# Optimization experiments

Measured on AMD Instinct MI355X. Metric: run time of the kernel, lower is better.

Reference implementation:

```python
import jax, jax.numpy as jnp
import numpy as np

C = 512
NUM_HEADS = 8
HEAD_DIM = C // NUM_HEADS


def setup_inputs() -> dict:
    key = jax.random.key(0)
    ks = jax.random.split(key, 5)
    B, H, W = 4, 48, 48
    x = jax.random.normal(ks[0], (B, C, H, W), dtype=jnp.float32)
    # 1x1 conv weights == dense matrices over channel dim
    Wqkv = jax.random.normal(ks[1], (3 * C, C), dtype=jnp.float32) * (1.0 / np.sqrt(C))
    bqkv = jax.random.normal(ks[2], (3 * C,), dtype=jnp.float32) * 0.01
    Wout = jax.random.normal(ks[3], (C, C), dtype=jnp.float32) * (1.0 / np.sqrt(C))
    bout = jax.random.normal(ks[4], (C,), dtype=jnp.float32) * 0.01
    return {"x": x, "Wqkv": Wqkv, "bqkv": bqkv, "Wout": Wout, "bout": bout}


def reference(x, Wqkv, bqkv, Wout, bout):
    B, Cc, H, W = x.shape
    S = H * W
    # qkv 1x1 conv: [B, 3C, H, W] -> reshape (B, 3, heads, head_dim, S)
    qkv = jnp.einsum('bchw,oc->bohw', x, Wqkv) + bqkv[None, :, None, None]
    qkv = qkv.reshape(B, 3, NUM_HEADS, HEAD_DIM, S)
    q, k, v = qkv[:, 0], qkv[:, 1], qkv[:, 2]  # [B, h, d, S]
    # tokens along S: q^T k, scaled softmax
    scale = HEAD_DIM ** -0.5
    attn = jnp.einsum('bhds,bhdt->bhst', q, k) * scale  # [B, h, S, S]
    attn = jax.nn.softmax(attn, axis=-1)
    out = jnp.einsum('bhst,bhdt->bhds', attn, v)  # [B, h, d, S]
    out = out.reshape(B, Cc, H, W)
    out = jnp.einsum('bchw,oc->bohw', out, Wout) + bout[None, :, None, None]
    return out
```

## Files before the change

kernel.cpp:

```cpp
#include <hip/hip_runtime.h>

#define S_LEN 2304
#define CDIM  512
#define NHEAD 8

typedef __attribute__((ext_vector_type(4)))  float f32x4;
typedef __attribute__((ext_vector_type(16))) float f32x16;
typedef __attribute__((ext_vector_type(8)))  _Float16 f16x8;
typedef __attribute__((ext_vector_type(2)))  __fp16 fp16x2r;
typedef _Float16 h16;

#define QSCALE 0.18033688011112042f

__device__ __forceinline__ float fexp2(float x) {
#if __has_builtin(__builtin_amdgcn_exp2f)
    return __builtin_amdgcn_exp2f(x);
#else
    return exp2f(x);
#endif
}

__device__ __forceinline__ unsigned cvtpk(float a, float b) {
    union { fp16x2r v; unsigned u; } c;
    c.v = __builtin_amdgcn_cvt_pkrtz(a, b);
    return c.u;
}

__device__ __forceinline__ void gll16(const h16* g, h16* l) {
    __builtin_amdgcn_global_load_lds(
        (const __attribute__((address_space(1))) unsigned int*)g,
        (__attribute__((address_space(3))) unsigned int*)l, 16, 0, 0);
}

__global__ __launch_bounds__(256) void xpose_x(
    const float* __restrict__ x, h16* __restrict__ xT)
{
    const int s0 = blockIdx.x * 64;
    const int c0 = blockIdx.y * 64;
    const int b  = blockIdx.z;
    __shared__ h16 Ts[64][76];

    const int t  = threadIdx.x;
    const int cq = t >> 4;
    const int sq = t & 15;

    const float* xb = x + ((size_t)b * CDIM + c0 + cq * 4) * S_LEN + s0 + sq * 4;
    float4 r0 = *(const float4*)(xb);
    float4 r1 = *(const float4*)(xb + S_LEN);
    float4 r2 = *(const float4*)(xb + 2 * S_LEN);
    float4 r3 = *(const float4*)(xb + 3 * S_LEN);

    union { h16 h[4]; uint2 u; } pk;
    pk.h[0]=(h16)r0.x; pk.h[1]=(h16)r1.x; pk.h[2]=(h16)r2.x; pk.h[3]=(h16)r3.x;
    *(uint2*)&Ts[sq*4+0][cq*4] = pk.u;
    pk.h[0]=(h16)r0.y; pk.h[1]=(h16)r1.y; pk.h[2]=(h16)r2.y; pk.h[3]=(h16)r3.y;
    *(uint2*)&Ts[sq*4+1][cq*4] = pk.u;
    pk.h[0]=(h16)r0.z; pk.h[1]=(h16)r1.z; pk.h[2]=(h16)r2.z; pk.h[3]=(h16)r3.z;
    *(uint2*)&Ts[sq*4+2][cq*4] = pk.u;
    pk.h[0]=(h16)r0.w; pk.h[1]=(h16)r1.w; pk.h[2]=(h16)r2.w; pk.h[3]=(h16)r3.w;
    *(uint2*)&Ts[sq*4+3][cq*4] = pk.u;

    __syncthreads();
    const int s  = t >> 2;
    const int cc = (t & 3) * 16;
    uint2 a0 = *(uint2*)&Ts[s][cc + 0];
    uint2 a1 = *(uint2*)&Ts[s][cc + 4];
    uint2 a2 = *(uint2*)&Ts[s][cc + 8];
    uint2 a3 = *(uint2*)&Ts[s][cc + 12];
    h16* dst = xT + ((size_t)b * S_LEN + s0 + s) * CDIM + c0 + cc;
    uint4 w0 = make_uint4(a0.x, a0.y, a1.x, a1.y);
    uint4 w1 = make_uint4(a2.x, a2.y, a3.x, a3.y);
    *(uint4*)dst       = w0;
    *(uint4*)(dst + 8) = w1;
}

__global__ __launch_bounds__(256) void wconv(
    const float* __restrict__ Wq, const float* __restrict__ Wo,
    h16* __restrict__ Wq_h, h16* __restrict__ Wo_h)
{
    const int NQ = 1536 * 512;
    const int NO = 512 * 512;
    int i = (blockIdx.x * 256 + threadIdx.x) * 4;
    if (i >= NQ + NO) return;
    float4 v;
    h16* dst;
    if (i < NQ) { v = *(const float4*)(Wq + i);        dst = Wq_h + i; }
    else        { v = *(const float4*)(Wo + (i - NQ)); dst = Wo_h + (i - NQ); }
    union { h16 h[4]; uint2 u; } pk;
    pk.h[0]=(h16)v.x; pk.h[1]=(h16)v.y; pk.h[2]=(h16)v.z; pk.h[3]=(h16)v.w;
    *(uint2*)dst = pk.u;
}

__global__ __launch_bounds__(256) void gemm_qkv(
    const h16* __restrict__ Wh, const float* __restrict__ bqkv,
    const h16* __restrict__ xT, h16* __restrict__ qT, h16* __restrict__ kT,
    h16* __restrict__ vN)
{
    const int n0 = blockIdx.x * 128;
    const int m0 = blockIdx.y * 128;
    const int b  = blockIdx.z;
    __shared__ h16 Ws[128 * 64];
    __shared__ h16 Xs[128 * 64];

    const int tid = threadIdx.x;
    const int lid = tid & 63, w = tid >> 6;
    const int g = lid >> 4, ln = lid & 15;
    const int wm = w & 1, wn = w >> 1;
    const int srow = lid >> 3;
    const int sblk = (lid & 7) ^ (srow & 7);

    f32x4 acc[4][4];
#pragma unroll
    for (int i = 0; i < 4; i++)
#pragma unroll
        for (int j = 0; j < 4; j++) acc[i][j] = (f32x4)0.f;

    const h16* Wbase = Wh + (size_t)m0 * CDIM;
    const h16* Xbase = xT + ((size_t)b * S_LEN + n0) * CDIM;
    const bool vblk = (m0 >= 1024);

    for (int kt = 0; kt < CDIM; kt += 64) {
        __syncthreads();
#pragma unroll
        for (int i = 0; i < 4; i++) {
            const int row0 = w * 32 + i * 8;
            gll16(Wbase + (size_t)(row0 + srow) * CDIM + kt + sblk * 8, &Ws[row0 * 64]);
            gll16(Xbase + (size_t)(row0 + srow) * CDIM + kt + sblk * 8, &Xs[row0 * 64]);
        }
        __syncthreads();

#pragma unroll
        for (int kc = 0; kc < 2; kc++) {
            f16x8 af[4], bf[4];
#pragma unroll
            for (int i = 0; i < 4; i++) {
                const int ra = wm * 64 + i * 16 + ln;
                const int ca = (kc * 64 + g * 16) ^ ((ra & 7) << 4);
                af[i] = *(const f16x8*)&Ws[ra * 64 + ca / 2];
                const int rb = wn * 64 + i * 16 + ln;
                const int cb = (kc * 64 + g * 16) ^ ((rb & 7) << 4);
                bf[i] = *(const f16x8*)&Xs[rb * 64 + cb / 2];
            }
            if (!vblk) {
#pragma unroll
                for (int i = 0; i < 4; i++)
#pragma unroll
                    for (int j = 0; j < 4; j++)
                        acc[i][j] = __builtin_amdgcn_mfma_f32_16x16x32_f16(
                            af[i], bf[j], acc[i][j], 0, 0, 0);
            } else {
#pragma unroll
                for (int i = 0; i < 4; i++)
#pragma unroll
                    for (int j = 0; j < 4; j++)
                        acc[i][j] = __builtin_amdgcn_mfma_f32_16x16x32_f16(
                            bf[i], af[j], acc[i][j], 0, 0, 0);
            }
        }
    }

    if (!vblk) {
#pragma unroll
        for (int i = 0; i < 4; i++) {
            const int mb = m0 + wm * 64 + i * 16 + 4 * g;
            const float4 bv = *(const float4*)&bqkv[mb];
            const int mloc = mb & 511;
            const int hh = mloc >> 6, d0 = mloc & 63;
            const bool isq = (mb < 512);
            const float scl = isq ? QSCALE : 1.0f;
            h16* base = (isq ? qT : kT);
#pragma unroll
            for (int j = 0; j < 4; j++) {
                const int n = n0 + wn * 64 + j * 16 + ln;
                union { h16 h[4]; uint2 u; } pk;
                pk.h[0] = (h16)((acc[i][j][0] + bv.x) * scl);
                pk.h[1] = (h16)((acc[i][j][1] + bv.y) * scl);
                pk.h[2] = (h16)((acc[i][j][2] + bv.z) * scl);
                pk.h[3] = (h16)((acc[i][j][3] + bv.w) * scl);
                *(uint2*)(base + (((size_t)b * 8 + hh) * S_LEN + n) * 64 + d0) = pk.u;
            }
        }
    } else {
#pragma unroll
        for (int j = 0; j < 4; j++) {
            const int m = m0 + wm * 64 + j * 16 + ln;
            const float bias = bqkv[m];
            const int mloc = m - 1024;
            const int hh = mloc >> 6, d = mloc & 63;
            h16* base = vN + (((size_t)b * 8 + hh) * 64 + d) * S_LEN;
#pragma unroll
            for (int i = 0; i < 4; i++) {
                const int nb = n0 + wn * 64 + i * 16 + 4 * g;
                union { h16 h[4]; uint2 u; } pk;
                pk.h[0] = (h16)(acc[i][j][0] + bias);
                pk.h[1] = (h16)(acc[i][j][1] + bias);
                pk.h[2] = (h16)(acc[i][j][2] + bias);
                pk.h[3] = (h16)(acc[i][j][3] + bias);
                *(uint2*)(base + nb) = pk.u;
            }
        }
    }
}

__global__ __launch_bounds__(256, 4) void attn_f16(
    const h16* __restrict__ qT, const h16* __restrict__ kT,
    const h16* __restrict__ vN, h16* __restrict__ attT)
{
    const int f    = blockIdx.x;
    const int xcd  = f & 7;
    const int slot = f >> 3;
    const int bh   = xcd + 8 * (slot / 18);
    const int x    = slot % 18;
    const int b    = bh >> 3;
    const int h    = bh & 7;
    const int s0   = x * 128;

    __shared__ h16 Ks[2][64 * 64];
    __shared__ h16 Vs[2][64 * 64];

    const int tid = threadIdx.x;
    const int lid = tid & 63, w = tid >> 6;
    const int l31 = lid & 31, hi = lid >> 5;
    const int srow = lid >> 3;
    const int sblk = (lid & 7) ^ (srow & 7);

    const h16* qb = qT + ((size_t)b * 8 + h) * S_LEN * 64;
    const h16* kb = kT + ((size_t)b * 8 + h) * S_LEN * 64;
    const h16* vb = vN + ((size_t)b * 8 + h) * 64 * S_LEN;

    const int sq = s0 + w * 32 + l31;

    f16x8 qf[4];
    {
        const h16* qrow = qb + (size_t)sq * 64;
#pragma unroll
        for (int ds = 0; ds < 4; ds++)
            qf[ds] = *(const f16x8*)(qrow + ds * 16 + hi * 8);
    }

    for (int c = w; c < 16; c += 4) {
        if (c < 8)
            gll16(kb + (size_t)(c * 8 + srow) * 64 + sblk * 8, &Ks[0][c * 8 * 64]);
        else
            gll16(vb + (size_t)((c - 8) * 8 + srow) * S_LEN + sblk * 8,
                  &Vs[0][(c - 8) * 8 * 64]);
    }
    __syncthreads();

    float m_run = -1e30f, l_run = 0.f;
    f32x16 oacc0 = (f32x16)0.f, oacc1 = (f32x16)0.f;

    int cur = 0;
    for (int kt = 0; kt < S_LEN; kt += 64, cur ^= 1) {
        if (kt + 64 < S_LEN) {
            for (int c = w; c < 16; c += 4) {
                if (c < 8)
                    gll16(kb + (size_t)(kt + 64 + c * 8 + srow) * 64 + sblk * 8,
                          &Ks[cur ^ 1][c * 8 * 64]);
                else
                    gll16(vb + (size_t)((c - 8) * 8 + srow) * S_LEN + kt + 64 + sblk * 8,
                          &Vs[cur ^ 1][(c - 8) * 8 * 64]);
            }
        }
        const h16* Kc = Ks[cur];
        const h16* Vc = Vs[cur];

        f32x16 sacc0 = (f32x16)0.f, sacc1 = (f32x16)0.f;
        __builtin_amdgcn_s_setprio(1);
#pragma unroll
        for (int ds = 0; ds < 4; ds++) {
            const int bc = 2 * ds + hi;
            {
                const int row = l31;
                f16x8 kf = *(const f16x8*)&Kc[row * 64 + ((bc ^ (row & 7)) * 8)];
                sacc0 = __builtin_amdgcn_mfma_f32_32x32x16_f16(kf, qf[ds], sacc0, 0, 0, 0);
            }
            {
                const int row = 32 + l31;
                f16x8 kf = *(const f16x8*)&Kc[row * 64 + ((bc ^ (row & 7)) * 8)];
                sacc1 = __builtin_amdgcn_mfma_f32_32x32x16_f16(kf, qf[ds], sacc1, 0, 0, 0);
            }
        }
        __builtin_amdgcn_s_setprio(0);

        float mloc = -1e30f;
#pragma unroll
        for (int r = 0; r < 16; r++) {
            mloc = fmaxf(mloc, sacc0[r]);
            mloc = fmaxf(mloc, sacc1[r]);
        }
        mloc = fmaxf(mloc, __shfl_xor(mloc, 32));

        if (!__all(mloc <= m_run + 8.0f)) {
            const float mnew = fmaxf(m_run, mloc);
            const float resc = fexp2(m_run - mnew);
#pragma unroll
            for (int r = 0; r < 16; r++) { oacc0[r] *= resc; oacc1[r] *= resc; }
            l_run *= resc;
            m_run = mnew;
        }

        float lsum = 0.f;
#pragma unroll
        for (int r = 0; r < 16; r++) {
            sacc0[r] = fexp2(sacc0[r] - m_run); lsum += sacc0[r];
        }
#pragma unroll
        for (int r = 0; r < 16; r++) {
            sacc1[r] = fexp2(sacc1[r] - m_run); lsum += sacc1[r];
        }
        l_run += lsum + __shfl_xor(lsum, 32);

        f16x8 pf[4];
#pragma unroll
        for (int i = 0; i < 4; i++) {
            const int bse = (i & 1) * 8;
            float pv[8];
#pragma unroll
            for (int r = 0; r < 8; r++)
                pv[r] = (i < 2) ? sacc0[bse + r] : sacc1[bse + r];
            unsigned X0 = cvtpk(pv[0], pv[1]);
            unsigned X1 = cvtpk(pv[2], pv[3]);
            unsigned Y0 = cvtpk(pv[4], pv[5]);
            unsigned Y1 = cvtpk(pv[6], pv[7]);
            asm("v_permlane32_swap_b32 %0, %1" : "+v"(X0), "+v"(Y0));
            asm("v_permlane32_swap_b32 %0, %1" : "+v"(X1), "+v"(Y1));
            union { unsigned u[4]; f16x8 v; } pkk;
            pkk.u[0] = X0; pkk.u[1] = X1; pkk.u[2] = Y0; pkk.u[3] = Y1;
            pf[i] = pkk.v;
        }

        __builtin_amdgcn_s_setprio(1);
#pragma unroll
        for (int i = 0; i < 4; i++) {
            const int bc = 2 * i + hi;
            {
                const int row = l31;
                f16x8 vf = *(const f16x8*)&Vc[row * 64 + ((bc ^ (row & 7)) * 8)];
                oacc0 = __builtin_amdgcn_mfma_f32_32x32x16_f16(vf, pf[i], oacc0, 0, 0, 0);
            }
            {
                const int row = 32 + l31;
                f16x8 vf = *(const f16x8*)&Vc[row * 64 + ((bc ^ (row & 7)) * 8)];
                oacc1 = __builtin_amdgcn_mfma_f32_32x32x16_f16(vf, pf[i], oacc1, 0, 0, 0);
            }
        }
        __builtin_amdgcn_s_setprio(0);
        __syncthreads();
    }

    const float inv = 1.0f / l_run;
    h16* ob = attT + ((size_t)b * S_LEN + sq) * CDIM + h * 64;
#pragma unroll
    for (int gi = 0; gi < 4; gi++) {
        union { h16 hh[4]; uint2 u; } p0, p1;
#pragma unroll
        for (int r = 0; r < 4; r++) {
            p0.hh[r] = (h16)(oacc0[gi * 4 + r] * inv);
            p1.hh[r] = (h16)(oacc1[gi * 4 + r] * inv);
        }
        *(uint2*)(ob + 8 * gi + 4 * hi)      = p0.u;
        *(uint2*)(ob + 32 + 8 * gi + 4 * hi) = p1.u;
    }
}

__global__ __launch_bounds__(256) void gemm_out(
    const h16* __restrict__ attT, const h16* __restrict__ Wh,
    const float* __restrict__ bout, float* __restrict__ out)
{
    const int n0 = blockIdx.x * 128;
    const int m0 = blockIdx.y * 128;
    const int b  = blockIdx.z;
    __shared__ h16 Ws[128 * 64];
    __shared__ h16 Xs[128 * 64];

    const int tid = threadIdx.x;
    const int lid = tid & 63, w = tid >> 6;
    const int g = lid >> 4, ln = lid & 15;
    const int wm = w & 1, wn = w >> 1;
    const int srow = lid >> 3;
    const int sblk = (lid & 7) ^ (srow & 7);

    f32x4 acc[4][4];
#pragma unroll
    for (int i = 0; i < 4; i++)
#pragma unroll
        for (int j = 0; j < 4; j++) acc[i][j] = (f32x4)0.f;

    const h16* Wbase = Wh + (size_t)m0 * CDIM;
    const h16* Xbase = attT + ((size_t)b * S_LEN + n0) * CDIM;

    for (int kt = 0; kt < CDIM; kt += 64) {
        __syncthreads();
#pragma unroll
        for (int i = 0; i < 4; i++) {
            const int row0 = w * 32 + i * 8;
            gll16(Wbase + (size_t)(row0 + srow) * CDIM + kt + sblk * 8, &Ws[row0 * 64]);
            gll16(Xbase + (size_t)(row0 + srow) * CDIM + kt + sblk * 8, &Xs[row0 * 64]);
        }
        __syncthreads();

#pragma unroll
        for (int kc = 0; kc < 2; kc++) {
            f16x8 af[4], bf[4];
#pragma unroll
            for (int i = 0; i < 4; i++) {
                const int ra = wm * 64 + i * 16 + ln;
                const int ca = (kc * 64 + g * 16) ^ ((ra & 7) << 4);
                af[i] = *(const f16x8*)&Ws[ra * 64 + ca / 2];
                const int rb = wn * 64 + i * 16 + ln;
                const int cb = (kc * 64 + g * 16) ^ ((rb & 7) << 4);
                bf[i] = *(const f16x8*)&Xs[rb * 64 + cb / 2];
            }
#pragma unroll
            for (int i = 0; i < 4; i++)
#pragma unroll
                for (int j = 0; j < 4; j++)
                    acc[i][j] = __builtin_amdgcn_mfma_f32_16x16x32_f16(
                        bf[i], af[j], acc[i][j], 0, 0, 0);
        }
    }

#pragma unroll
    for (int j = 0; j < 4; j++) {
        const int m = m0 + wm * 64 + j * 16 + ln;
        const float bias = bout[m];
        float* base = out + ((size_t)b * CDIM + m) * S_LEN;
#pragma unroll
        for (int i = 0; i < 4; i++) {
            const int nb = n0 + wn * 64 + i * 16 + 4 * g;
            float4 o;
            o.x = acc[i][j][0] + bias;
            o.y = acc[i][j][1] + bias;
            o.z = acc[i][j][2] + bias;
            o.w = acc[i][j][3] + bias;
            *(float4*)(base + nb) = o;
        }
    }
}

extern "C" void kernel_launch(void* const* d_in, const int* in_sizes, int n_in,
                              void* d_out, int out_size, void* d_ws, size_t ws_size,
                              hipStream_t stream)
{
    const float* x    = (const float*)d_in[0];
    const float* Wqkv = (const float*)d_in[1];
    const float* bqkv = (const float*)d_in[2];
    const float* Wout = (const float*)d_in[3];
    const float* bout = (const float*)d_in[4];
    float* out = (float*)d_out;

    h16* xT   = (h16*)d_ws;
    h16* Wq_h = xT   + (size_t)4 * S_LEN * CDIM;
    h16* Wo_h = Wq_h + (size_t)1536 * 512;
    h16* qT   = Wo_h + (size_t)512 * 512;
    h16* kT   = qT   + (size_t)4 * 8 * S_LEN * 64;
    h16* vN   = kT   + (size_t)4 * 8 * S_LEN * 64;
    h16* attT = vN   + (size_t)4 * 8 * S_LEN * 64;

    xpose_x <<<dim3(36, 8, 4),  256, 0, stream>>>(x, xT);
    wconv   <<<1024,            256, 0, stream>>>(Wqkv, Wout, Wq_h, Wo_h);
    gemm_qkv<<<dim3(18, 12, 4), 256, 0, stream>>>(Wq_h, bqkv, xT, qT, kT, vN);
    attn_f16<<<576,             256, 0, stream>>>(qT, kT, vN, attT);
    gemm_out<<<dim3(18, 4, 4),  256, 0, stream>>>(attT, Wo_h, bout, out);
}
```

Baseline: 137.8 us.

## Use 3-wave attention blocks, 768 blocks, and compute row sums via MFMA

Attention blocks shrink from 4 to 3 waves (96 queries each), and the grid grows to 768 blocks with a matching XCD mapping. The goal is better balance of work across compute units. The softmax denominator now comes from an extra MFMA against a ones vector instead of VALU adds plus a cross-lane shuffle, and the max reduction is restructured into two independent chains. Fewer waves each load more of the K/V tile, and the extra MFMA adds matrix-core work and accumulator registers.

Result: no change. 136.6 us (-0.9%).

```diff
diff --git a/kernel.cpp b/kernel.cpp
--- a/kernel.cpp
+++ b/kernel.cpp
@@ -202,18 +202,18 @@
     }
 }
 
-__global__ __launch_bounds__(256, 4) void attn_f16(
+__global__ __launch_bounds__(192, 4) void attn_f16(
     const h16* __restrict__ qT, const h16* __restrict__ kT,
     const h16* __restrict__ vN, h16* __restrict__ attT)
 {
     const int f    = blockIdx.x;
     const int xcd  = f & 7;
     const int slot = f >> 3;
-    const int bh   = xcd + 8 * (slot / 18);
-    const int x    = slot % 18;
+    const int bh   = xcd + 8 * (slot / 24);
+    const int x    = slot % 24;
     const int b    = bh >> 3;
     const int h    = bh & 7;
-    const int s0   = x * 128;
+    const int s0   = x * 96;
 
     __shared__ h16 Ks[2][64 * 64];
     __shared__ h16 Vs[2][64 * 64];
@@ -238,7 +238,11 @@
             qf[ds] = *(const f16x8*)(qrow + ds * 16 + hi * 8);
     }
 
-    for (int c = w; c < 16; c += 4) {
+    f16x8 ones;
+#pragma unroll
+    for (int i = 0; i < 8; i++) ones[i] = (h16)1.0f;
+
+    for (int c = w; c < 16; c += 3) {
         if (c < 8)
             gll16(kb + (size_t)(c * 8 + srow) * 64 + sblk * 8, &Ks[0][c * 8 * 64]);
         else
@@ -247,13 +251,13 @@
     }
     __syncthreads();
 
-    float m_run = -1e30f, l_run = 0.f;
-    f32x16 oacc0 = (f32x16)0.f, oacc1 = (f32x16)0.f;
+    float m_run = -1e30f;
+    f32x16 oacc0 = (f32x16)0.f, oacc1 = (f32x16)0.f, lacc = (f32x16)0.f;
 
     int cur = 0;
     for (int kt = 0; kt < S_LEN; kt += 64, cur ^= 1) {
         if (kt + 64 < S_LEN) {
-            for (int c = w; c < 16; c += 4) {
+            for (int c = w; c < 16; c += 3) {
                 if (c < 8)
                     gll16(kb + (size_t)(kt + 64 + c * 8 + srow) * 64 + sblk * 8,
                           &Ks[cur ^ 1][c * 8 * 64]);
@@ -283,33 +287,31 @@
         }
         __builtin_amdgcn_s_setprio(0);
 
-        float mloc = -1e30f;
-#pragma unroll
-        for (int r = 0; r < 16; r++) {
-            mloc = fmaxf(mloc, sacc0[r]);
-            mloc = fmaxf(mloc, sacc1[r]);
-        }
+        float ma = sacc0[0], mb2 = sacc1[0];
+#pragma unroll
+        for (int r = 1; r < 15; r += 2) {
+            ma  = fmaxf(fmaxf(ma,  sacc0[r]), sacc0[r + 1]);
+            mb2 = fmaxf(fmaxf(mb2, sacc1[r]), sacc1[r + 1]);
+        }
+        ma  = fmaxf(ma,  sacc0[15]);
+        mb2 = fmaxf(mb2, sacc1[15]);
+        float mloc = fmaxf(ma, mb2);
         mloc = fmaxf(mloc, __shfl_xor(mloc, 32));
 
         if (!__all(mloc <= m_run + 8.0f)) {
             const float mnew = fmaxf(m_run, mloc);
             const float resc = fexp2(m_run - mnew);
 #pragma unroll
-            for (int r = 0; r < 16; r++) { oacc0[r] *= resc; oacc1[r] *= resc; }
-            l_run *= resc;
+            for (int r = 0; r < 16; r++) {
+                oacc0[r] *= resc; oacc1[r] *= resc; lacc[r] *= resc;
+            }
             m_run = mnew;
         }
 
-        float lsum = 0.f;
-#pragma unroll
-        for (int r = 0; r < 16; r++) {
-            sacc0[r] = fexp2(sacc0[r] - m_run); lsum += sacc0[r];
-        }
-#pragma unroll
-        for (int r = 0; r < 16; r++) {
-            sacc1[r] = fexp2(sacc1[r] - m_run); lsum += sacc1[r];
-        }
-        l_run += lsum + __shfl_xor(lsum, 32);
+#pragma unroll
+        for (int r = 0; r < 16; r++) sacc0[r] = fexp2(sacc0[r] - m_run);
+#pragma unroll
+        for (int r = 0; r < 16; r++) sacc1[r] = fexp2(sacc1[r] - m_run);
 
         f16x8 pf[4];
 #pragma unroll
@@ -334,6 +336,7 @@
 #pragma unroll
         for (int i = 0; i < 4; i++) {
             const int bc = 2 * i + hi;
+            lacc = __builtin_amdgcn_mfma_f32_32x32x16_f16(ones, pf[i], lacc, 0, 0, 0);
             {
                 const int row = l31;
                 f16x8 vf = *(const f16x8*)&Vc[row * 64 + ((bc ^ (row & 7)) * 8)];
@@ -349,7 +352,7 @@
         __syncthreads();
     }
 
-    const float inv = 1.0f / l_run;
+    const float inv = 1.0f / lacc[0];
     h16* ob = attT + ((size_t)b * S_LEN + sq) * CDIM + h * 64;
 #pragma unroll
     for (int gi = 0; gi < 4; gi++) {
@@ -461,6 +464,6 @@
     xpose_x <<<dim3(36, 8, 4),  256, 0, stream>>>(x, xT);
     wconv   <<<1024,            256, 0, stream>>>(Wqkv, Wout, Wq_h, Wo_h);
     gemm_qkv<<<dim3(18, 12, 4), 256, 0, stream>>>(Wq_h, bqkv, xT, qT, kT, vN);
-    attn_f16<<<576,             256, 0, stream>>>(qT, kT, vN, attT);
+    attn_f16<<<768,             192, 0, stream>>>(qT, kT, vN, attT);
     gemm_out<<<dim3(18, 4, 4),  256, 0, stream>>>(attT, Wo_h, bout, out);
 }
```
